# Kernel tuning notes

Measured on AMD Instinct MI355X. Metric: run time of the kernel, lower is better.

## Reference

```python
import jax, jax.numpy as jnp
import numpy as np

N = 8192        # nodes
D_IN = 256      # in_dims
D_OUT = 32      # out_dims (assignment clusters)


def setup_inputs() -> dict:
    key = jax.random.key(0)
    k1, k2, k3 = jax.random.split(key, 3)
    main_feat = jax.random.normal(k1, (N, D_IN), dtype=jnp.float32)
    main_adj = jax.random.uniform(k2, (N, N), dtype=jnp.float32)
    W = jax.random.normal(k3, (D_IN, D_OUT), dtype=jnp.float32) * (1.0 / np.sqrt(D_IN))
    b = jnp.zeros((D_OUT,), dtype=jnp.float32)
    return {"main_feat": main_feat, "main_adj": main_adj, "W": W, "b": b}


def reference(main_feat, main_adj, W, b):
    # GraphConvolution: support = X @ W ; out = A @ support + b   -> [N, D_OUT]
    support = main_feat @ W
    assign = main_adj @ support + b
    # softmax over the NODE axis (dim 0), matching F.softmax(main_assign, 0)
    assign = jax.nn.softmax(assign, axis=0)
    # pooling: raw_emb = assign^T @ X  -> [D_OUT, D_IN]
    raw_emb = assign.T @ main_feat
    return raw_emb
```

## Files before the change

### kernel.cpp

```cpp
#include <hip/hip_runtime.h>
#include <stdint.h>

#define NN   8192
#define DIN  256
#define DOUT 32

#define PP4   (DOUT * DIN + 320)

typedef short bf16x8 __attribute__((ext_vector_type(8)));
typedef float f32x16 __attribute__((ext_vector_type(16)));

union BF8 { uint32_t u[4]; bf16x8 v; };

__device__ __forceinline__ void split_pair(float a, float b, uint32_t& hp, uint32_t& lp) {
    uint32_t ua = __float_as_uint(a), ub = __float_as_uint(b);
    hp = (ua >> 16) | (ub & 0xffff0000u);
    float la = a - __uint_as_float(ua & 0xffff0000u);
    float lb = b - __uint_as_float(ub & 0xffff0000u);
    lp = (__float_as_uint(la) >> 16) | (__float_as_uint(lb) & 0xffff0000u);
}

__global__ __launch_bounds__(256) void k1_support(
    const float* __restrict__ X, const float* __restrict__ W,
    unsigned short* __restrict__ hi_frag, unsigned short* __restrict__ lo_frag)
{
    __shared__ float Xs[32 * 256];
    int t = threadIdx.x;
    int kbase = blockIdx.x * 32;

    const float4* Xg = (const float4*)(X + (size_t)kbase * DIN);
    float4* Xs4 = (float4*)Xs;
#pragma unroll
    for (int p = 0; p < 8; ++p) Xs4[p * 256 + t] = Xg[p * 256 + t];
    __syncthreads();

    int c = t & 31;
    int q = t >> 5;
    int kb2  = q >> 2;
    int half = (q >> 1) & 1;
    int j4   = q & 1;
    int krow0 = kb2 * 16 + half * 8 + j4 * 4;

    float acc[4] = {0.f, 0.f, 0.f, 0.f};
    for (int d = 0; d < 256; ++d) {
        float w = W[d * 32 + c];
#pragma unroll
        for (int jj = 0; jj < 4; ++jj)
            acc[jj] += Xs[(krow0 + jj) * 256 + d] * w;
    }

    uint32_t h01, l01, h23, l23;
    split_pair(acc[0], acc[1], h01, l01);
    split_pair(acc[2], acc[3], h23, l23);

    int ks = (kbase >> 4) + kb2;
    size_t elembase = (size_t)ks * 512 + (size_t)(half * 32 + c) * 8 + j4 * 4;
    *(uint2*)(hi_frag + elembase) = make_uint2(h01, h23);
    *(uint2*)(lo_frag + elembase) = make_uint2(l01, l23);
}

__global__ __launch_bounds__(512) void k2_logits(
    const float* __restrict__ adj,
    const unsigned short* __restrict__ hi_frag,
    const unsigned short* __restrict__ lo_frag,
    float* __restrict__ part)
{
    __shared__ float red[8 * 1088];
    int t = threadIdx.x;
    int lane = t & 63, wv = t >> 6;
    int row0 = blockIdx.x * 32;
    int y = blockIdx.y;
    int r  = lane & 31;
    int hs = lane >> 5;

    const float* arow = adj + (size_t)(row0 + r) * NN + y * 4096 + wv * 512 + hs * 8;
    const unsigned short* hp = hi_frag + ((size_t)y * 256 + wv * 32) * 512 + lane * 8;
    const unsigned short* lp = lo_frag + ((size_t)y * 256 + wv * 32) * 512 + lane * 8;

    f32x16 acc;
#pragma unroll
    for (int i = 0; i < 16; ++i) acc[i] = 0.f;

#pragma unroll 4
    for (int s = 0; s < 32; ++s) {
        float4 a0 = *(const float4*)arow;
        float4 a1 = *(const float4*)(arow + 4);
        BF8 bh, bl, ah, al;
        bh.v = *(const bf16x8*)hp;
        bl.v = *(const bf16x8*)lp;
        split_pair(a0.x, a0.y, ah.u[0], al.u[0]);
        split_pair(a0.z, a0.w, ah.u[1], al.u[1]);
        split_pair(a1.x, a1.y, ah.u[2], al.u[2]);
        split_pair(a1.z, a1.w, ah.u[3], al.u[3]);
        acc = __builtin_amdgcn_mfma_f32_32x32x16_bf16(ah.v, bh.v, acc, 0, 0, 0);
        acc = __builtin_amdgcn_mfma_f32_32x32x16_bf16(ah.v, bl.v, acc, 0, 0, 0);
        acc = __builtin_amdgcn_mfma_f32_32x32x16_bf16(al.v, bh.v, acc, 0, 0, 0);
        arow += 16; hp += 512; lp += 512;
    }

#pragma unroll
    for (int g = 0; g < 16; ++g) red[wv * 1088 + lane * 17 + g] = acc[g];
    __syncthreads();

    float* pdst = part + (size_t)y * (NN * DOUT) + (size_t)row0 * 32;
    for (int a = t; a < 1024; a += 512) {
        int row = a >> 5, col = a & 31;
        int l = col + 32 * ((row >> 2) & 1);
        int g = (row & 3) | ((row >> 3) << 2);
        float ssum = 0.f;
#pragma unroll
        for (int w8 = 0; w8 < 8; ++w8) ssum += red[w8 * 1088 + l * 17 + g];
        pdst[a] = ssum;
    }
}

__global__ __launch_bounds__(256) void t1_sum_max(
    const float* __restrict__ part, float* __restrict__ logits_sum,
    float* __restrict__ Mpart)
{
    __shared__ float red[256 * 4];
    int t = threadIdx.x;
    size_t f = (size_t)blockIdx.x * 256 + t;

    float4 v = ((const float4*)part)[f];
    {
        float4 u = ((const float4*)(part + (size_t)NN * DOUT))[f];
        v.x += u.x; v.y += u.y; v.z += u.z; v.w += u.w;
    }
    ((float4*)logits_sum)[f] = v;

    red[t * 4 + 0] = v.x; red[t * 4 + 1] = v.y;
    red[t * 4 + 2] = v.z; red[t * 4 + 3] = v.w;
    __syncthreads();
    for (int s = 128; s >= 8; s >>= 1) {
        if (t < s)
#pragma unroll
            for (int j = 0; j < 4; ++j)
                red[t * 4 + j] = fmaxf(red[t * 4 + j], red[(t + s) * 4 + j]);
        __syncthreads();
    }
    if (t < 8)
#pragma unroll
        for (int j = 0; j < 4; ++j)
            Mpart[blockIdx.x * 32 + t * 4 + j] = red[t * 4 + j];
}

__global__ __launch_bounds__(256) void t2_exp_pool(
    const float* __restrict__ logits_sum, const float* __restrict__ Mpart,
    const float* __restrict__ X, float* __restrict__ Spart,
    float* __restrict__ p4)
{
    __shared__ float red[256 * 4];
    __shared__ float As[32 * 32];
    __shared__ float Xs[8 * 256];
    int t = threadIdx.x;
    int b = blockIdx.x;
    int c = t & 31, g0 = t >> 5;

    {
        float m = -3.4e38f;
#pragma unroll
        for (int gg = 0; gg < 32; ++gg)
            m = fmaxf(m, Mpart[(g0 * 32 + gg) * 32 + c]);
        red[t] = m;
    }
    __syncthreads();
    for (int s = 128; s >= 32; s >>= 1) {
        if (t < s) red[t] = fmaxf(red[t], red[t + s]);
        __syncthreads();
    }
    float m0 = red[(4 * t + 0) & 31], m1 = red[(4 * t + 1) & 31];
    float m2 = red[(4 * t + 2) & 31], m3 = red[(4 * t + 3) & 31];
    __syncthreads();

    size_t f = (size_t)b * 256 + t;
    float4 v = ((const float4*)logits_sum)[f];
    v.x = __expf(v.x - m0); v.y = __expf(v.y - m1);
    v.z = __expf(v.z - m2); v.w = __expf(v.w - m3);
    {
        int row = t >> 3, cb = (4 * t) & 31;
        As[row * 32 + cb]     = v.x;
        As[row * 32 + cb + 1] = v.y;
        As[row * 32 + cb + 2] = v.z;
        As[row * 32 + cb + 3] = v.w;
    }
    red[t * 4 + 0] = v.x; red[t * 4 + 1] = v.y;
    red[t * 4 + 2] = v.z; red[t * 4 + 3] = v.w;
    __syncthreads();
    for (int s = 128; s >= 8; s >>= 1) {
        if (t < s)
#pragma unroll
            for (int j = 0; j < 4; ++j)
                red[t * 4 + j] += red[(t + s) * 4 + j];
        __syncthreads();
    }
    if (t < 8)
#pragma unroll
        for (int j = 0; j < 4; ++j)
            Spart[b * 32 + t * 4 + j] = red[t * 4 + j];

    int dg = t >> 5;
    int ibase = b * 32;
    float acc[32];
#pragma unroll
    for (int i = 0; i < 32; ++i) acc[i] = 0.f;

    for (int rnd = 0; rnd < 4; ++rnd) {
        __syncthreads();
        const float4* Xg = (const float4*)(X + (size_t)(ibase + rnd * 8) * DIN);
        float4* Xs4 = (float4*)Xs;
        Xs4[t]       = Xg[t];
        Xs4[256 + t] = Xg[256 + t];
        __syncthreads();
#pragma unroll
        for (int i2 = 0; i2 < 8; ++i2) {
            float a = As[(rnd * 8 + i2) * 32 + c];
#pragma unroll
            for (int dd = 0; dd < 32; ++dd)
                acc[dd] += a * Xs[i2 * 256 + dg * 32 + dd];
        }
    }
    float* dst = p4 + (size_t)b * PP4 + (size_t)c * 256 + dg * 32;
#pragma unroll
    for (int q = 0; q < 8; ++q)
        ((float4*)dst)[q] = make_float4(acc[q * 4], acc[q * 4 + 1],
                                        acc[q * 4 + 2], acc[q * 4 + 3]);
}

__global__ __launch_bounds__(256) void t3_reduce(
    const float* __restrict__ p4, const float* __restrict__ Spart,
    float* __restrict__ out)
{
    __shared__ float red[256];
    __shared__ float sred[256];
    int t = threadIdx.x;
    int c_out = blockIdx.x >> 3;

    sred[t] = Spart[t * 32 + c_out];

    int j = blockIdx.x * 32 + (t & 31);
    int g0 = t >> 5;
    float a = 0.f;
#pragma unroll
    for (int gg = 0; gg < 32; ++gg) {
        int g = (g0 * 32 + gg + blockIdx.x) & 255;
        a += p4[(size_t)g * PP4 + j];
    }
    red[t] = a;
    __syncthreads();
    for (int s = 128; s >= 32; s >>= 1) {
        if (t < s) { red[t] += red[t + s]; sred[t] += sred[t + s]; }
        __syncthreads();
    }
    if (t < 32) {
        float sv = sred[t];
#pragma unroll
        for (int off = 16; off >= 1; off >>= 1) sv += __shfl_xor(sv, off);
        out[blockIdx.x * 32 + t] = red[t] / sv;
    }
}

extern "C" void kernel_launch(void* const* d_in, const int* in_sizes, int n_in,
                              void* d_out, int out_size, void* d_ws, size_t ws_size,
                              hipStream_t stream) {
    const float* X   = (const float*)d_in[0];
    const float* adj = (const float*)d_in[1];
    const float* W   = (const float*)d_in[2];
    float* out = (float*)d_out;

    char* w = (char*)d_ws;
    unsigned short* hi_frag = (unsigned short*)w;
    unsigned short* lo_frag = (unsigned short*)(w + 512 * 1024);
    size_t off = 1024 * 1024;
    float* part = (float*)(w + off);        off += (size_t)2 * NN * DOUT * sizeof(float);
    float* logits_sum = (float*)(w + off);  off += (size_t)NN * DOUT * sizeof(float);
    float* Mpart = (float*)(w + off);       off += 256 * 32 * sizeof(float);
    float* Spart = (float*)(w + off);       off += 256 * 32 * sizeof(float);
    float* p4 = (float*)(w + off);          off += (size_t)256 * PP4 * sizeof(float);

    k1_support<<<NN / 32, 256, 0, stream>>>(X, W, hi_frag, lo_frag);
    k2_logits<<<dim3(NN / 32, 2), 512, 0, stream>>>(adj, hi_frag, lo_frag, part);
    t1_sum_max<<<256, 256, 0, stream>>>(part, logits_sum, Mpart);
    t2_exp_pool<<<256, 256, 0, stream>>>(logits_sum, Mpart, X, Spart, p4);
    t3_reduce<<<256, 256, 0, stream>>>(p4, Spart, out);
}
```

Before: 416.2 us.

## Drop split-K in logits kernel and fuse column max into it

The adjacency GEMM kernel no longer splits the K dimension across two grid slices. Each block now covers the full 8192-long row segment, with each wave taking 1024 columns and running twice as many iterations. Because each block produces final logits, the separate sum/max kernel is removed: the block writes logits_sum directly and does the per-block column max in shared memory. This saves a kernel launch and the partial-buffer round trip, but halves the grid to 256 blocks, which lowers parallelism for the memory-bound adjacency stream.

```diff
diff --git a/kernel.cpp b/kernel.cpp
--- a/kernel.cpp
+++ b/kernel.cpp
@@ -63,26 +63,27 @@
     const float* __restrict__ adj,
     const unsigned short* __restrict__ hi_frag,
     const unsigned short* __restrict__ lo_frag,
-    float* __restrict__ part)
+    float* __restrict__ logits_sum,
+    float* __restrict__ Mpart)
 {
     __shared__ float red[8 * 1088];
     int t = threadIdx.x;
     int lane = t & 63, wv = t >> 6;
-    int row0 = blockIdx.x * 32;
-    int y = blockIdx.y;
+    int b = blockIdx.x;
+    int row0 = b * 32;
     int r  = lane & 31;
     int hs = lane >> 5;
 
-    const float* arow = adj + (size_t)(row0 + r) * NN + y * 4096 + wv * 512 + hs * 8;
-    const unsigned short* hp = hi_frag + ((size_t)y * 256 + wv * 32) * 512 + lane * 8;
-    const unsigned short* lp = lo_frag + ((size_t)y * 256 + wv * 32) * 512 + lane * 8;
+    const float* arow = adj + (size_t)(row0 + r) * NN + wv * 1024 + hs * 8;
+    const unsigned short* hp = hi_frag + (size_t)(wv * 64) * 512 + lane * 8;
+    const unsigned short* lp = lo_frag + (size_t)(wv * 64) * 512 + lane * 8;
 
     f32x16 acc;
 #pragma unroll
     for (int i = 0; i < 16; ++i) acc[i] = 0.f;
 
-#pragma unroll 4
-    for (int s = 0; s < 32; ++s) {
+#pragma unroll 8
+    for (int s = 0; s < 64; ++s) {
         float4 a0 = *(const float4*)arow;
         float4 a1 = *(const float4*)(arow + 4);
         BF8 bh, bl, ah, al;
@@ -102,47 +103,29 @@
     for (int g = 0; g < 16; ++g) red[wv * 1088 + lane * 17 + g] = acc[g];
     __syncthreads();
 
-    float* pdst = part + (size_t)y * (NN * DOUT) + (size_t)row0 * 32;
-    for (int a = t; a < 1024; a += 512) {
+    float vout[2];
+#pragma unroll
+    for (int e = 0; e < 2; ++e) {
+        int a = t + e * 512;
         int row = a >> 5, col = a & 31;
         int l = col + 32 * ((row >> 2) & 1);
         int g = (row & 3) | ((row >> 3) << 2);
         float ssum = 0.f;
 #pragma unroll
         for (int w8 = 0; w8 < 8; ++w8) ssum += red[w8 * 1088 + l * 17 + g];
-        pdst[a] = ssum;
-    }
-}
-
-__global__ __launch_bounds__(256) void t1_sum_max(
-    const float* __restrict__ part, float* __restrict__ logits_sum,
-    float* __restrict__ Mpart)
-{
-    __shared__ float red[256 * 4];
-    int t = threadIdx.x;
-    size_t f = (size_t)blockIdx.x * 256 + t;
-
-    float4 v = ((const float4*)part)[f];
-    {
-        float4 u = ((const float4*)(part + (size_t)NN * DOUT))[f];
-        v.x += u.x; v.y += u.y; v.z += u.z; v.w += u.w;
-    }
-    ((float4*)logits_sum)[f] = v;
-
-    red[t * 4 + 0] = v.x; red[t * 4 + 1] = v.y;
-    red[t * 4 + 2] = v.z; red[t * 4 + 3] = v.w;
-    __syncthreads();
-    for (int s = 128; s >= 8; s >>= 1) {
-        if (t < s)
-#pragma unroll
-            for (int j = 0; j < 4; ++j)
-                red[t * 4 + j] = fmaxf(red[t * 4 + j], red[(t + s) * 4 + j]);
-        __syncthreads();
-    }
-    if (t < 8)
-#pragma unroll
-        for (int j = 0; j < 4; ++j)
-            Mpart[blockIdx.x * 32 + t * 4 + j] = red[t * 4 + j];
+        logits_sum[(size_t)b * 1024 + a] = ssum;
+        vout[e] = ssum;
+    }
+
+    float mx2 = fmaxf(vout[0], vout[1]);
+    __syncthreads();
+    red[t] = mx2;
+    __syncthreads();
+    for (int s = 256; s >= 32; s >>= 1) {
+        if (t < s) red[t] = fmaxf(red[t], red[t + s]);
+        __syncthreads();
+    }
+    if (t < 32) Mpart[b * 32 + t] = red[t];
 }
 
 __global__ __launch_bounds__(256) void t2_exp_pool(
@@ -272,15 +255,13 @@
     unsigned short* hi_frag = (unsigned short*)w;
     unsigned short* lo_frag = (unsigned short*)(w + 512 * 1024);
     size_t off = 1024 * 1024;
-    float* part = (float*)(w + off);        off += (size_t)2 * NN * DOUT * sizeof(float);
     float* logits_sum = (float*)(w + off);  off += (size_t)NN * DOUT * sizeof(float);
     float* Mpart = (float*)(w + off);       off += 256 * 32 * sizeof(float);
     float* Spart = (float*)(w + off);       off += 256 * 32 * sizeof(float);
     float* p4 = (float*)(w + off);          off += (size_t)256 * PP4 * sizeof(float);
 
     k1_support<<<NN / 32, 256, 0, stream>>>(X, W, hi_frag, lo_frag);
-    k2_logits<<<dim3(NN / 32, 2), 512, 0, stream>>>(adj, hi_frag, lo_frag, part);
-    t1_sum_max<<<256, 256, 0, stream>>>(part, logits_sum, Mpart);
+    k2_logits<<<NN / 32, 512, 0, stream>>>(adj, hi_frag, lo_frag, logits_sum, Mpart);
     t2_exp_pool<<<256, 256, 0, stream>>>(logits_sum, Mpart, X, Spart, p4);
     t3_reduce<<<256, 256, 0, stream>>>(p4, Spart, out);
 }
```

Measured after the change: 431.3 us. 3.6% more time.
